# Performance work log

Measured on AMD Instinct MI355X. Metric: run time of the kernel, lower is better.

## Reference

```python
import jax, jax.numpy as jnp
import numpy as np

N_NODES = 200000
N_EDGES = 400000
N_GRAPHS = 4096
IN_DIM, HID_DIM, OUT_DIM, EDGE_DIM = 128, 256, 256, 16


def setup_inputs() -> dict:
    key = jax.random.key(0)
    ks = jax.random.split(key, 16)
    x = jax.random.normal(ks[0], (N_NODES, IN_DIM), dtype=jnp.float32)
    edge_attr = jax.random.normal(ks[1], (N_EDGES, EDGE_DIM), dtype=jnp.float32)
    edge_index = jax.random.randint(ks[2], (2, N_EDGES), 0, N_NODES, dtype=jnp.int64)
    batch = jnp.sort(jax.random.randint(ks[3], (N_NODES,), 0, N_GRAPHS, dtype=jnp.int64))

    def lin(k, fan_in, fan_out):
        bound = 1.0 / np.sqrt(fan_in)
        kw, kb = jax.random.split(k)
        W = jax.random.uniform(kw, (fan_in, fan_out), minval=-bound, maxval=bound, dtype=jnp.float32)
        b = jax.random.uniform(kb, (fan_out,), minval=-bound, maxval=bound, dtype=jnp.float32)
        return W, b

    We1, be1 = lin(ks[4], EDGE_DIM, IN_DIM)    # GINEConv1 edge projection
    W1a, b1a = lin(ks[5], IN_DIM, HID_DIM)     # conv1 MLP layer 1
    W1b, b1b = lin(ks[6], HID_DIM, HID_DIM)    # conv1 MLP layer 2
    We2, be2 = lin(ks[7], EDGE_DIM, HID_DIM)   # GINEConv2 edge projection
    W2a, b2a = lin(ks[8], HID_DIM, HID_DIM)    # conv2 MLP layer 1
    W2b, b2b = lin(ks[9], HID_DIM, OUT_DIM)    # conv2 MLP layer 2
    return {"x": x, "edge_attr": edge_attr,
            "We1": We1, "be1": be1, "W1a": W1a, "b1a": b1a, "W1b": W1b, "b1b": b1b,
            "We2": We2, "be2": be2, "W2a": W2a, "b2a": b2a, "W2b": W2b, "b2b": b2b,
            "edge_index": edge_index, "batch": batch}


def _gine_conv(x, edge_attr, src, dst, We, be, Wa, ba, Wb, bb):
    # messages: relu(x_j + lin_edge(e)), scatter-add into destination nodes
    e_proj = edge_attr @ We + be                      # [E, D]
    msg = jax.nn.relu(x[src] + e_proj)                # [E, D]
    aggr = jax.ops.segment_sum(msg, dst, num_segments=x.shape[0])  # [N, D]
    h = x + aggr                                      # (1 + eps) * x_i + aggr, eps=0
    h = jax.nn.relu(h @ Wa + ba)
    return h @ Wb + bb


def reference(x, edge_attr, We1, be1, W1a, b1a, W1b, b1b,
              We2, be2, W2a, b2a, W2b, b2b, edge_index, batch):
    src, dst = edge_index[0], edge_index[1]
    h = jax.nn.relu(_gine_conv(x, edge_attr, src, dst, We1, be1, W1a, b1a, W1b, b1b))
    h = jax.nn.relu(_gine_conv(h, edge_attr, src, dst, We2, be2, W2a, b2a, W2b, b2b))
    # global mean pool over graphs
    sums = jax.ops.segment_sum(h, batch, num_segments=N_GRAPHS)            # [G, D]
    counts = jax.ops.segment_sum(jnp.ones((h.shape[0],), h.dtype), batch,
                                 num_segments=N_GRAPHS)                    # [G]
    return sums / jnp.maximum(counts, 1.0)[:, None]
```

## Files before the change

### kernel.cpp

```cpp
#include <hip/hip_runtime.h>
#include <hip/hip_bf16.h>

typedef float f32x4 __attribute__((ext_vector_type(4)));
typedef float f32x2 __attribute__((ext_vector_type(2)));
typedef unsigned short u16x2 __attribute__((ext_vector_type(2)));
typedef unsigned short u16x4 __attribute__((ext_vector_type(4)));
typedef unsigned short u16x8 __attribute__((ext_vector_type(8)));
typedef short s16x8 __attribute__((ext_vector_type(8)));

#define NN 200000
#define NE 400000
#define NG 4096
#define SCHUNK 1024
#define NSCAN ((NN + SCHUNK - 1) / SCHUNK)

template<int C> struct VecT;
template<> struct VecT<2> { using T = u16x2; };
template<> struct VecT<4> { using T = u16x4; };

__device__ __forceinline__ unsigned short f2bf(float f) {
    union { float f; unsigned int u; } v; v.f = f;
    unsigned int r = v.u + 0x7FFF + ((v.u >> 16) & 1);
    return (unsigned short)(r >> 16);
}
__device__ __forceinline__ float bf2f(unsigned short b) {
    union { unsigned int u; float f; } v; v.u = ((unsigned int)b) << 16;
    return v.f;
}

__global__ void detect_i64(const int* __restrict__ ei, int* __restrict__ flag) {
    unsigned long long m = __ballot(ei[threadIdx.x * 2 + 1] == 0);
    if (threadIdx.x == 0) *flag = (~m == 0ULL) ? 1 : 0;
}
__device__ __forceinline__ int load_idx(const int* p, long long i, int f64) {
    return f64 ? (int)((const long long*)p)[i] : p[i];
}

__global__ __launch_bounds__(256) void bat_conv(const int* __restrict__ bat,
                                                const int* __restrict__ flag,
                                                int* __restrict__ bat32) {
    int i = blockIdx.x * 256 + threadIdx.x;
    if (i < NN) bat32[i] = *flag ? (int)((const long long*)bat)[i] : bat[i];
}

__global__ void wt_conv(const float* __restrict__ W, unsigned short* __restrict__ Wt,
                        int K, int N) {
    int tid = blockIdx.x * 256 + threadIdx.x;
    if (tid >= K * N) return;
    int n = tid / K, k = tid - n * K;
    Wt[tid] = f2bf(W[(size_t)k * N + n]);
}

__global__ __launch_bounds__(256) void x2bf(const float* __restrict__ x,
                                            unsigned short* __restrict__ xh) {
    long long i = ((long long)blockIdx.x * 256 + threadIdx.x) * 4;
    if (i >= (long long)NN * 128) return;
    f32x4 v = *(const f32x4*)(x + i);
    u16x4 o; o.x = f2bf(v.x); o.y = f2bf(v.y); o.z = f2bf(v.z); o.w = f2bf(v.w);
    *(u16x4*)(xh + i) = o;
}

__global__ __launch_bounds__(256) void ea_perm(const float* __restrict__ ea,
                                               const int* __restrict__ eidx,
                                               const int* __restrict__ totE_p,
                                               float* __restrict__ eac) {
    int j = blockIdx.x * 256 + threadIdx.x;
    if (j >= *totE_p) return;
    int e = eidx[j];
    if ((unsigned)e >= NE) e = 0;
    const float* s = ea + (size_t)e * 16;
    float* d = eac + (size_t)j * 16;
#pragma unroll
    for (int k = 0; k < 4; ++k)
        *(f32x4*)(d + k * 4) = *(const f32x4*)(s + k * 4);
}

__global__ __launch_bounds__(256) void hist_dst(const int* __restrict__ ei,
                                                const int* __restrict__ flag,
                                                int* __restrict__ deg) {
    int e = blockIdx.x * 256 + threadIdx.x;
    if (e >= NE) return;
    int f64 = *flag;
    int s = load_idx(ei, e, f64);
    int d = load_idx(ei, (long long)NE + e, f64);
    if ((unsigned)s < NN && (unsigned)d < NN) atomicAdd(&deg[d], 1);
}

__global__ __launch_bounds__(256) void scan_bsum(const int* __restrict__ deg,
                                                 int* __restrict__ bsum) {
    __shared__ int red[256];
    int t = threadIdx.x, base = blockIdx.x * SCHUNK + t * 4;
    int s = 0;
#pragma unroll
    for (int c = 0; c < 4; ++c) { int i = base + c; if (i < NN) s += deg[i]; }
    red[t] = s; __syncthreads();
    for (int o = 128; o > 0; o >>= 1) { if (t < o) red[t] += red[t + o]; __syncthreads(); }
    if (t == 0) bsum[blockIdx.x] = red[0];
}

__global__ void scan_carry(int* __restrict__ bsum, int* __restrict__ rowptr_end) {
    if (threadIdx.x == 0) {
        int run = 0;
        for (int i = 0; i < NSCAN; ++i) { int v = bsum[i]; bsum[i] = run; run += v; }
        *rowptr_end = run;
    }
}

__global__ __launch_bounds__(256) void scan_final(const int* __restrict__ deg,
                                                  const int* __restrict__ bsum,
                                                  int* __restrict__ rowptr,
                                                  int* __restrict__ cursor) {
    __shared__ int lds[256];
    int t = threadIdx.x, base = blockIdx.x * SCHUNK + t * 4;
    int v[4], s = 0;
#pragma unroll
    for (int c = 0; c < 4; ++c) { int i = base + c; v[c] = (i < NN) ? deg[i] : 0; s += v[c]; }
    lds[t] = s; __syncthreads();
    for (int o = 1; o < 256; o <<= 1) {
        int x = 0;
        if (t >= o) x = lds[t - o];
        __syncthreads();
        if (t >= o) lds[t] += x;
        __syncthreads();
    }
    int run = lds[t] - s + bsum[blockIdx.x];
#pragma unroll
    for (int c = 0; c < 4; ++c) {
        int i = base + c;
        if (i < NN) { rowptr[i] = run; cursor[i] = run; }
        run += v[c];
    }
}

__global__ __launch_bounds__(256) void fill_csr(const int* __restrict__ ei,
                                                const int* __restrict__ flag,
                                                int* __restrict__ cursor,
                                                int* __restrict__ srcs,
                                                int* __restrict__ eidx) {
    int e = blockIdx.x * 256 + threadIdx.x;
    if (e >= NE) return;
    int f64 = *flag;
    int s = load_idx(ei, e, f64);
    int d = load_idx(ei, (long long)NE + e, f64);
    if ((unsigned)s >= NN || (unsigned)d >= NN) return;
    int pos = atomicAdd(&cursor[d], 1);
    if ((unsigned)pos < NE) { srcs[pos] = s; eidx[pos] = e; }
}

template<int C, int U>
__global__ __launch_bounds__(256)
void msg_build(const unsigned short* __restrict__ xh,
               const float* __restrict__ eac,
               const float* __restrict__ We, const float* __restrict__ be,
               const int* __restrict__ srcs, const int* __restrict__ totE_p,
               unsigned short* __restrict__ M) {
    using XV = typename VecT<C>::T;
    constexpr int D = 64 * C;
    constexpr int C2 = C / 2;
    const int wid  = (blockIdx.x * 256 + threadIdx.x) >> 6;
    const int lane = threadIdx.x & 63;
    const int totE = *totE_p;
    const int col = lane * C;

    f32x2 w2[16][C2], bb2[C2];
#pragma unroll
    for (int k = 0; k < 16; ++k)
#pragma unroll
        for (int c = 0; c < C2; ++c)
            w2[k][c] = *(const f32x2*)(We + k * D + col + 2 * c);
#pragma unroll
    for (int c = 0; c < C2; ++c) bb2[c] = *(const f32x2*)(be + col + 2 * c);

    const int j0 = wid * U;
    int sv[U];
    XV xv[U];
#pragma unroll
    for (int u = 0; u < U; ++u) {
        int j = j0 + u;
        sv[u] = (j < totE) ? srcs[j] : -1;
    }
#pragma unroll
    for (int u = 0; u < U; ++u) {
        if ((unsigned)sv[u] < NN)
            xv[u] = *(const XV*)(xh + (size_t)sv[u] * D + col);
        else
            xv[u] = (XV)0;
    }
#pragma unroll
    for (int u = 0; u < U; ++u) {
        int j = j0 + u;
        if (j >= totE) continue;
        const float* eap = eac + (size_t)j * 16;
        f32x4 e0 = *(const f32x4*)eap;
        f32x4 e1 = *(const f32x4*)(eap + 4);
        f32x4 e2 = *(const f32x4*)(eap + 8);
        f32x4 e3 = *(const f32x4*)(eap + 12);
        f32x2 m2[C2];
#pragma unroll
        for (int c = 0; c < C2; ++c) {
            f32x2 xx; xx.x = bf2f(xv[u][2 * c]); xx.y = bf2f(xv[u][2 * c + 1]);
            m2[c] = bb2[c] + xx;
        }
#pragma unroll
        for (int k = 0; k < 4; ++k) {
            f32x2 k0; k0.x = e0[k]; k0.y = e0[k];
            f32x2 k1; k1.x = e1[k]; k1.y = e1[k];
            f32x2 k2; k2.x = e2[k]; k2.y = e2[k];
            f32x2 k3; k3.x = e3[k]; k3.y = e3[k];
#pragma unroll
            for (int c = 0; c < C2; ++c) {
                m2[c] += k0 * w2[k][c];
                m2[c] += k1 * w2[4 + k][c];
                m2[c] += k2 * w2[8 + k][c];
                m2[c] += k3 * w2[12 + k][c];
            }
        }
        XV o;
#pragma unroll
        for (int c = 0; c < C2; ++c) {
            o[2 * c]     = f2bf(fmaxf(m2[c].x, 0.f));
            o[2 * c + 1] = f2bf(fmaxf(m2[c].y, 0.f));
        }
        *(XV*)(M + (size_t)j * D + col) = o;
    }
}

template<int C>
__global__ __launch_bounds__(256)
void seg_sum(const unsigned short* __restrict__ M, const int* __restrict__ rowptr,
             const unsigned short* __restrict__ self, unsigned short* __restrict__ outp) {
    using XV = typename VecT<C>::T;
    constexpr int D = 64 * C;
    const int node = (blockIdx.x * 256 + threadIdx.x) >> 6;
    const int lane = threadIdx.x & 63;
    if (node >= NN) return;
    const int col = lane * C;
    int lo = rowptr[node], hi = rowptr[node + 1];
    if (lo > hi || (unsigned)hi > NE) { lo = 0; hi = 0; }

    float a[C];
    XV sv = *(const XV*)(self + (size_t)node * D + col);
#pragma unroll
    for (int c = 0; c < C; ++c) a[c] = bf2f(sv[c]);

    int j = lo;
    for (; j + 1 < hi; j += 2) {
        XV m0 = *(const XV*)(M + (size_t)j * D + col);
        XV m1 = *(const XV*)(M + (size_t)(j + 1) * D + col);
#pragma unroll
        for (int c = 0; c < C; ++c) a[c] += bf2f(m0[c]) + bf2f(m1[c]);
    }
    if (j < hi) {
        XV m0 = *(const XV*)(M + (size_t)j * D + col);
#pragma unroll
        for (int c = 0; c < C; ++c) a[c] += bf2f(m0[c]);
    }
    XV o;
#pragma unroll
    for (int c = 0; c < C; ++c) o[c] = f2bf(a[c]);
    *(XV*)(outp + (size_t)node * D + col) = o;
}

template<int K1, int MODE>
__global__ __launch_bounds__(256, 3)
void gemm2_fused(const unsigned short* __restrict__ A,
                 const unsigned short* __restrict__ Wta, const float* __restrict__ ba,
                 const unsigned short* __restrict__ Wtb, const float* __restrict__ bb,
                 unsigned short* __restrict__ C,
                 float* __restrict__ sums, const int* __restrict__ bat32) {
    constexpr int LDA = K1 + 4;
    constexpr int LDM = 260;
    constexpr int P1 = K1 / 32;
    constexpr int NC = P1 + 8;
    __shared__ unsigned short Us[64 * LDM];
    const int m0 = blockIdx.x * 64;
    const int tid = threadIdx.x;
    const int wave = tid >> 6;
    const int lane = tid & 63;
    const int lm = lane & 15;
    const int lq = lane >> 4;
    const int nw = wave * 64;

    {
        const int arow = tid >> 2;
        const int acol = (tid & 3) * 8;
        const unsigned short* src = A + (size_t)(m0 + arow) * K1;
        unsigned short* dst = Us + arow * LDA;
#pragma unroll
        for (int c = 0; c < K1 / 32; ++c)
            *(u16x8*)(dst + acol + c * 32) = *(const u16x8*)(src + acol + c * 32);
    }

    auto ldbc = [&](int c, s16x8* bf) {
        if (c >= NC) return;
        const unsigned short* W = (c < P1) ? Wta : Wtb;
        const int KW = (c < P1) ? K1 : 256;
        const int k0 = (c < P1) ? c * 32 : (c - P1) * 32;
#pragma unroll
        for (int nt = 0; nt < 4; ++nt)
            bf[nt] = *(const s16x8*)(W + (size_t)(nw + nt * 16 + lm) * KW + k0 + lq * 8);
    };

    f32x4 acc[4][4] = {};
    s16x8 b0[4], b1[4], b2[4];

    ldbc(0, b0);
    ldbc(1, b1);
    __syncthreads();

#pragma unroll
    for (int i = 0; i < P1; ++i) {
        ldbc(i + 2, b2);
        const int k0 = i * 32;
        s16x8 af[4];
#pragma unroll
        for (int mt = 0; mt < 4; ++mt)
            af[mt] = *(const s16x8*)(Us + (mt * 16 + lm) * LDA + k0 + lq * 8);
#pragma unroll
        for (int mt = 0; mt < 4; ++mt)
#pragma unroll
            for (int nt = 0; nt < 4; ++nt)
                acc[mt][nt] = __builtin_amdgcn_mfma_f32_16x16x32_bf16(
                    af[mt], b0[nt], acc[mt][nt], 0, 0, 0);
#pragma unroll
        for (int nt = 0; nt < 4; ++nt) { b0[nt] = b1[nt]; b1[nt] = b2[nt]; }
    }

    __syncthreads();

#pragma unroll
    for (int mt = 0; mt < 4; ++mt) {
        const int row = mt * 16 + lq * 4;
#pragma unroll
        for (int nt = 0; nt < 4; ++nt) {
            int coln = nw + nt * 16 + lm;
            float bv = ba[coln];
#pragma unroll
            for (int r = 0; r < 4; ++r) {
                float v = fmaxf(acc[mt][nt][r] + bv, 0.f);
                Us[(row + r) * LDM + coln] = f2bf(v);
                acc[mt][nt][r] = 0.f;
            }
        }
    }
    __syncthreads();

#pragma unroll
    for (int j = 0; j < 8; ++j) {
        ldbc(P1 + j + 2, b2);
        const int k0 = j * 32;
        s16x8 af[4];
#pragma unroll
        for (int mt = 0; mt < 4; ++mt)
            af[mt] = *(const s16x8*)(Us + (mt * 16 + lm) * LDM + k0 + lq * 8);
#pragma unroll
        for (int mt = 0; mt < 4; ++mt)
#pragma unroll
            for (int nt = 0; nt < 4; ++nt)
                acc[mt][nt] = __builtin_amdgcn_mfma_f32_16x16x32_bf16(
                    af[mt], b0[nt], acc[mt][nt], 0, 0, 0);
#pragma unroll
        for (int nt = 0; nt < 4; ++nt) { b0[nt] = b1[nt]; b1[nt] = b2[nt]; }
    }

    if constexpr (MODE == 0) {
#pragma unroll
        for (int mt = 0; mt < 4; ++mt) {
            const int row = m0 + mt * 16 + lq * 4;
#pragma unroll
            for (int nt = 0; nt < 4; ++nt) {
                int coln = nw + nt * 16 + lm;
                float bv = bb[coln];
#pragma unroll
                for (int r = 0; r < 4; ++r) {
                    float v = fmaxf(acc[mt][nt][r] + bv, 0.f);
                    C[(size_t)(row + r) * 256 + coln] = f2bf(v);
                }
            }
        }
    } else {
        int g16[16];
#pragma unroll
        for (int mt = 0; mt < 4; ++mt)
#pragma unroll
            for (int r = 0; r < 4; ++r)
                g16[mt * 4 + r] = bat32[m0 + mt * 16 + lq * 4 + r];
#pragma unroll
        for (int nt = 0; nt < 4; ++nt) {
            int coln = nw + nt * 16 + lm;
            float bv = bb[coln];
            int curg = g16[0];
            float s = 0.f;
#pragma unroll
            for (int i = 0; i < 16; ++i) {
                float v = fmaxf(acc[i >> 2][nt][i & 3] + bv, 0.f);
                if (g16[i] != curg) {
                    if ((unsigned)curg < NG) atomicAdd(&sums[(size_t)curg * 256 + coln], s);
                    curg = g16[i]; s = 0.f;
                }
                s += v;
            }
            if ((unsigned)curg < NG) atomicAdd(&sums[(size_t)curg * 256 + coln], s);
        }
    }
}

__global__ __launch_bounds__(256)
void pool_div(const float* __restrict__ sums, const int* __restrict__ bat32,
              float* __restrict__ out) {
    int g = blockIdx.x;
    int a = 0, b = NN;
    while (a < b) { int m = (a + b) >> 1; if (bat32[m] < g) a = m + 1; else b = m; }
    int lo = a;
    b = NN;
    while (a < b) { int m = (a + b) >> 1; if (bat32[m] < g + 1) a = m + 1; else b = m; }
    float inv = 1.f / fmaxf((float)(a - lo), 1.f);
    out[(size_t)g * 256 + threadIdx.x] = sums[(size_t)g * 256 + threadIdx.x] * inv;
}

extern "C" void kernel_launch(void* const* d_in, const int* in_sizes, int n_in,
                              void* d_out, int out_size, void* d_ws, size_t ws_size,
                              hipStream_t stream) {
    const float* x   = (const float*)d_in[0];
    const float* ea  = (const float*)d_in[1];
    const float* We1 = (const float*)d_in[2];
    const float* be1 = (const float*)d_in[3];
    const float* W1a = (const float*)d_in[4];
    const float* b1a = (const float*)d_in[5];
    const float* W1b = (const float*)d_in[6];
    const float* b1b = (const float*)d_in[7];
    const float* We2 = (const float*)d_in[8];
    const float* be2 = (const float*)d_in[9];
    const float* W2a = (const float*)d_in[10];
    const float* b2a = (const float*)d_in[11];
    const float* W2b = (const float*)d_in[12];
    const float* b2b = (const float*)d_in[13];
    const int*   ei  = (const int*)d_in[14];
    const int*   bat = (const int*)d_in[15];
    float* out = (float*)d_out;

    char* ws = (char*)d_ws;
    const size_t SZH = (size_t)NN * 256 * 2;
    unsigned short* A  = (unsigned short*)ws;
    unsigned short* B  = (unsigned short*)(ws + SZH);
    char* Dr = ws + 3 * SZH;
    char* q = Dr;
    int* deg    = (int*)q; q += (size_t)NN * 4;
    int* rowptr = (int*)q; q += (size_t)(NN + 1) * 4;
    int* cursor = (int*)q; q += (size_t)NN * 4;
    int* srcs   = (int*)q; q += (size_t)NE * 4;
    int* eidx   = (int*)q; q += (size_t)NE * 4;
    int* bsum   = (int*)q; q += (size_t)NSCAN * 4;
    q = Dr + ((q - Dr + 63) & ~63ll);
    float*          eac = (float*)q; q += (size_t)NE * 16 * 4;
    unsigned short* xh  = (unsigned short*)q; q += (size_t)NN * 128 * 2;
    int*   bat32 = (int*)q;   q += (size_t)NN * 4;
    float* sums  = (float*)q; q += (size_t)NG * 256 * 4;
    char* p = ws + 4 * SZH;
    unsigned short* Wt1a = (unsigned short*)p; p += 128 * 256 * 2;
    unsigned short* Wt1b = (unsigned short*)p; p += 256 * 256 * 2;
    unsigned short* Wt2a = (unsigned short*)p; p += 256 * 256 * 2;
    unsigned short* Wt2b = (unsigned short*)p; p += 256 * 256 * 2;
    int* flag = (int*)p;

    detect_i64<<<1, 64, 0, stream>>>(ei, flag);
    bat_conv<<<(NN + 255) / 256, 256, 0, stream>>>(bat, flag, bat32);
    wt_conv<<<(128 * 256 + 255) / 256, 256, 0, stream>>>(W1a, Wt1a, 128, 256);
    wt_conv<<<(256 * 256 + 255) / 256, 256, 0, stream>>>(W1b, Wt1b, 256, 256);
    wt_conv<<<(256 * 256 + 255) / 256, 256, 0, stream>>>(W2a, Wt2a, 256, 256);
    wt_conv<<<(256 * 256 + 255) / 256, 256, 0, stream>>>(W2b, Wt2b, 256, 256);

    hipMemsetAsync(deg, 0, (size_t)NN * 4, stream);
    hipMemsetAsync(sums, 0, (size_t)NG * 256 * 4, stream);
    hist_dst<<<(NE + 255) / 256, 256, 0, stream>>>(ei, flag, deg);
    scan_bsum<<<NSCAN, 256, 0, stream>>>(deg, bsum);
    scan_carry<<<1, 64, 0, stream>>>(bsum, rowptr + NN);
    scan_final<<<NSCAN, 256, 0, stream>>>(deg, bsum, rowptr, cursor);
    fill_csr<<<(NE + 255) / 256, 256, 0, stream>>>(ei, flag, cursor, srcs, eidx);
    ea_perm<<<(NE + 255) / 256, 256, 0, stream>>>(ea, eidx, rowptr + NN, eac);
    x2bf<<<(NN * 128 / 4 + 255) / 256, 256, 0, stream>>>(x, xh);

    const int GM_BLK = NE / 32;
    const int GS_BLK = NN / 4;
    const int GG_BLK = NN / 64;

    msg_build<2, 8><<<GM_BLK, 256, 0, stream>>>(xh, eac, We1, be1, srcs, rowptr + NN, A);
    seg_sum<2><<<GS_BLK, 256, 0, stream>>>(A, rowptr, xh, B);
    gemm2_fused<128, 0><<<GG_BLK, 256, 0, stream>>>(B, Wt1a, b1a, Wt1b, b1b, A,
                                                    nullptr, nullptr);

    msg_build<4, 8><<<GM_BLK, 256, 0, stream>>>(A, eac, We2, be2, srcs, rowptr + NN, B);
    seg_sum<4><<<GS_BLK, 256, 0, stream>>>(B, rowptr, A, A);
    gemm2_fused<256, 1><<<GG_BLK, 256, 0, stream>>>(A, Wt2a, b2a, Wt2b, b2b, nullptr,
                                                    sums, bat32);

    pool_div<<<NG, 256, 0, stream>>>(sums, bat32, out);
}
```

Baseline: 844.8 us.

## Parallelize scan carry, deepen GEMM weight prefetch, enlarge msg_build edges per block

Measured after the change: 855.1 us. Within noise of the previous version (+1.2%).

```diff
diff --git a/kernel.cpp b/kernel.cpp
--- a/kernel.cpp
+++ b/kernel.cpp
@@ -98,12 +98,21 @@
     if (t == 0) bsum[blockIdx.x] = red[0];
 }
 
-__global__ void scan_carry(int* __restrict__ bsum, int* __restrict__ rowptr_end) {
-    if (threadIdx.x == 0) {
-        int run = 0;
-        for (int i = 0; i < NSCAN; ++i) { int v = bsum[i]; bsum[i] = run; run += v; }
-        *rowptr_end = run;
-    }
+__global__ __launch_bounds__(256) void scan_carry(int* __restrict__ bsum,
+                                                  int* __restrict__ rowptr_end) {
+    __shared__ int lds[256];
+    int t = threadIdx.x;
+    int v = (t < NSCAN) ? bsum[t] : 0;
+    lds[t] = v; __syncthreads();
+    for (int o = 1; o < 256; o <<= 1) {
+        int x = 0;
+        if (t >= o) x = lds[t - o];
+        __syncthreads();
+        if (t >= o) lds[t] += x;
+        __syncthreads();
+    }
+    if (t < NSCAN) bsum[t] = lds[t] - v;
+    if (t == 255) *rowptr_end = lds[255];
 }
 
 __global__ __launch_bounds__(256) void scan_final(const int* __restrict__ deg,
@@ -302,15 +311,16 @@
     };
 
     f32x4 acc[4][4] = {};
-    s16x8 b0[4], b1[4], b2[4];
+    s16x8 b0[4], b1[4], b2[4], b3[4];
 
     ldbc(0, b0);
     ldbc(1, b1);
+    ldbc(2, b2);
     __syncthreads();
 
 #pragma unroll
     for (int i = 0; i < P1; ++i) {
-        ldbc(i + 2, b2);
+        ldbc(i + 3, b3);
         const int k0 = i * 32;
         s16x8 af[4];
 #pragma unroll
@@ -323,7 +333,7 @@
                 acc[mt][nt] = __builtin_amdgcn_mfma_f32_16x16x32_bf16(
                     af[mt], b0[nt], acc[mt][nt], 0, 0, 0);
 #pragma unroll
-        for (int nt = 0; nt < 4; ++nt) { b0[nt] = b1[nt]; b1[nt] = b2[nt]; }
+        for (int nt = 0; nt < 4; ++nt) { b0[nt] = b1[nt]; b1[nt] = b2[nt]; b2[nt] = b3[nt]; }
     }
 
     __syncthreads();
@@ -347,7 +357,7 @@
 
 #pragma unroll
     for (int j = 0; j < 8; ++j) {
-        ldbc(P1 + j + 2, b2);
+        ldbc(P1 + j + 3, b3);
         const int k0 = j * 32;
         s16x8 af[4];
 #pragma unroll
@@ -360,7 +370,7 @@
                 acc[mt][nt] = __builtin_amdgcn_mfma_f32_16x16x32_bf16(
                     af[mt], b0[nt], acc[mt][nt], 0, 0, 0);
 #pragma unroll
-        for (int nt = 0; nt < 4; ++nt) { b0[nt] = b1[nt]; b1[nt] = b2[nt]; }
+        for (int nt = 0; nt < 4; ++nt) { b0[nt] = b1[nt]; b1[nt] = b2[nt]; b2[nt] = b3[nt]; }
     }
 
     if constexpr (MODE == 0) {
@@ -474,22 +484,22 @@
     hipMemsetAsync(sums, 0, (size_t)NG * 256 * 4, stream);
     hist_dst<<<(NE + 255) / 256, 256, 0, stream>>>(ei, flag, deg);
     scan_bsum<<<NSCAN, 256, 0, stream>>>(deg, bsum);
-    scan_carry<<<1, 64, 0, stream>>>(bsum, rowptr + NN);
+    scan_carry<<<1, 256, 0, stream>>>(bsum, rowptr + NN);
     scan_final<<<NSCAN, 256, 0, stream>>>(deg, bsum, rowptr, cursor);
     fill_csr<<<(NE + 255) / 256, 256, 0, stream>>>(ei, flag, cursor, srcs, eidx);
     ea_perm<<<(NE + 255) / 256, 256, 0, stream>>>(ea, eidx, rowptr + NN, eac);
     x2bf<<<(NN * 128 / 4 + 255) / 256, 256, 0, stream>>>(x, xh);
 
-    const int GM_BLK = NE / 32;
+    const int GM_BLK = (NE + 47) / 48;
     const int GS_BLK = NN / 4;
     const int GG_BLK = NN / 64;
 
-    msg_build<2, 8><<<GM_BLK, 256, 0, stream>>>(xh, eac, We1, be1, srcs, rowptr + NN, A);
+    msg_build<2, 12><<<GM_BLK, 256, 0, stream>>>(xh, eac, We1, be1, srcs, rowptr + NN, A);
     seg_sum<2><<<GS_BLK, 256, 0, stream>>>(A, rowptr, xh, B);
     gemm2_fused<128, 0><<<GG_BLK, 256, 0, stream>>>(B, Wt1a, b1a, Wt1b, b1b, A,
                                                     nullptr, nullptr);
 
-    msg_build<4, 8><<<GM_BLK, 256, 0, stream>>>(A, eac, We2, be2, srcs, rowptr + NN, B);
+    msg_build<4, 12><<<GM_BLK, 256, 0, stream>>>(A, eac, We2, be2, srcs, rowptr + NN, B);
     seg_sum<4><<<GS_BLK, 256, 0, stream>>>(B, rowptr, A, A);
     gemm2_fused<256, 1><<<GG_BLK, 256, 0, stream>>>(A, Wt2a, b2a, Wt2b, b2b, nullptr,
                                                     sums, bat32);
```
